# Kernel optimization log

Measured on AMD Instinct MI355X. Metric: run time of the kernel, lower is better.

The kernel has to match this reference:

```python
import jax, jax.numpy as jnp
import numpy as np

BCE_W, AMP_W, SMOOTH_W = 1.0, 0.5, 0.3
BIG = 1e30  # finite sentinel for masked min/max (avoids inf-inf NaNs)


def setup_inputs() -> dict:
    key = jax.random.key(0)
    k1, k2, k3 = jax.random.split(key, 3)
    B, L = 128, 100000
    signals = jax.random.normal(k1, (B, 1, L), dtype=jnp.float32)
    predictions = jax.random.normal(k2, (B, L, 1), dtype=jnp.float32)
    targets = jax.random.uniform(k3, (B, L, 1), dtype=jnp.float32)
    return {"signals": signals, "predictions": predictions, "targets": targets}


def _window_amp(mask, s, idx, L):
    # mask: [B, L] bool; s: [B, L] signal. Amplitude of s over [min_idx, max_idx].
    lo = jnp.min(jnp.where(mask, idx, L), axis=1)    # [B]
    hi = jnp.max(jnp.where(mask, idx, -1), axis=1)   # [B]
    w = (idx[None, :] >= lo[:, None]) & (idx[None, :] <= hi[:, None])  # [B, L]
    amp = jnp.max(jnp.where(w, s, -BIG), axis=1) - jnp.min(jnp.where(w, s, BIG), axis=1)
    return amp, jnp.any(mask, axis=1)


def reference(signals, predictions, targets):
    # predictions/targets: [B, L, 1] (3D path of the torch module)
    p, t = predictions, targets
    pred_sigmoid = jax.nn.sigmoid(p)
    # BCEWithLogitsLoss (mean), numerically stable
    bce_loss = jnp.mean(jnp.maximum(p, 0.0) - p * t + jnp.log1p(jnp.exp(-jnp.abs(p))))

    B, L = signals.shape[0], signals.shape[2]
    s = signals[:, 0, :]                              # [B, L]
    idx = jnp.arange(L)

    true_amp, t_has = _window_amp(t[:, :, 0] > 0.5, s, idx, L)
    pred_amp, p_has = _window_amp(pred_sigmoid[:, :, 0] > 0.5, s, idx, L)
    valid = t_has & p_has

    d = jnp.abs(true_amp - pred_amp)
    per = jnp.where(true_amp > 1e-6, d / (true_amp + 1e-6), d)
    amp_loss = jnp.sum(jnp.where(valid, per, 0.0)) / B

    # smoothness: mean |diff(pred_sigmoid, axis=1)|; L >= 2 so never empty
    smoothness_loss = jnp.mean(jnp.abs(pred_sigmoid[:, 1:, :] - pred_sigmoid[:, :-1, :]))

    return BCE_W * bce_loss + AMP_W * amp_loss + SMOOTH_W * smoothness_loss
```

## Files before the change

kernel.cpp:

```cpp
#include <hip/hip_runtime.h>
#include <math.h>
#include <float.h>

#define BATCH 128
#define LEN   100000
#define CHUNK 5000
#define SEGS  (LEN / CHUNK)
#define VPS   (CHUNK / 4)

struct WS {
    int*   lt_tab; int* ht_tab; int* lp_tab; int* hp_tab;
    float* bce_blk; float* sm_blk;
    float* cmin; float* cmax;
    float* wmn; float* wmx;
};

static inline WS ws_layout(void* d_ws) {
    WS w;
    w.lt_tab  = (int*)d_ws;
    w.ht_tab  = w.lt_tab + BATCH * SEGS;
    w.lp_tab  = w.ht_tab + BATCH * SEGS;
    w.hp_tab  = w.lp_tab + BATCH * SEGS;
    w.bce_blk = (float*)(w.hp_tab + BATCH * SEGS);
    w.sm_blk  = w.bce_blk + BATCH * SEGS;
    w.cmin    = w.sm_blk  + BATCH * SEGS;
    w.cmax    = w.cmin    + BATCH * SEGS;
    w.wmn     = w.cmax    + BATCH * SEGS;
    w.wmx     = w.wmn     + 2 * BATCH;
    return w;
}


__global__ __launch_bounds__(256) void k_main(
        const float* __restrict__ sig,
        const float* __restrict__ pred,
        const float* __restrict__ targ,
        int* __restrict__ lt_tab, int* __restrict__ ht_tab,
        int* __restrict__ lp_tab, int* __restrict__ hp_tab,
        float* __restrict__ bce_blk, float* __restrict__ sm_blk,
        float* __restrict__ cmin_tab, float* __restrict__ cmax_tab) {
    const int b   = blockIdx.y;
    const int seg = blockIdx.x;
    const int tid = threadIdx.x;
    const size_t row = (size_t)b * LEN;
    const float* prow = pred + row;
    const float* trow = targ + row;
    const float* srow = sig  + row;
    const int seg0 = seg * CHUNK;

    float bce = 0.0f, sm = 0.0f;
    float cmn = FLT_MAX, cmx = -FLT_MAX;
    int lt = LEN, ht = -1, lp = LEN, hp = -1;

    auto proc = [&](const float4& pv, const float4& tv, const float4& sv, int l0) {
        float sg0, sg1, sg2, sg3;
        #define ONE_ELEM(pp, tt, ss, sgv, ll) { \
            const float ap = fabsf(pp); \
            const float ee = __expf(-ap); \
            const float zz = 1.0f + ee; \
            const float rr = __builtin_amdgcn_rcpf(zz); \
            bce += fmaxf(pp, 0.0f) - (pp) * (tt) + __logf(zz); \
            sgv = ((pp) >= 0.0f) ? rr : ee * rr; \
            if ((tt) > 0.5f) { lt = min(lt, (ll)); ht = max(ht, (ll)); } \
            if ((pp) > 0.0f) { lp = min(lp, (ll)); hp = max(hp, (ll)); } \
            cmn = fminf(cmn, (ss)); cmx = fmaxf(cmx, (ss)); }
        ONE_ELEM(pv.x, tv.x, sv.x, sg0, l0 + 0)
        ONE_ELEM(pv.y, tv.y, sv.y, sg1, l0 + 1)
        ONE_ELEM(pv.z, tv.z, sv.z, sg2, l0 + 2)
        ONE_ELEM(pv.w, tv.w, sv.w, sg3, l0 + 3)
        #undef ONE_ELEM
        sm += fabsf(sg1 - sg0) + fabsf(sg2 - sg1) + fabsf(sg3 - sg2);
        const float prev3 = __shfl_up(sg3, 1);
        if ((tid & 63) == 0) {
            if (l0 > 0) {
                const float pp = prow[l0 - 1];
                const float ee = __expf(-fabsf(pp));
                const float rr = __builtin_amdgcn_rcpf(1.0f + ee);
                const float sp = (pp >= 0.0f) ? rr : ee * rr;
                sm += fabsf(sg0 - sp);
            }
        } else {
            sm += fabsf(sg0 - prev3);
        }
    };

    for (int vv = tid; vv < VPS; vv += 512) {
        const int l0 = seg0 + vv * 4;
        const float4 pv0 = *reinterpret_cast<const float4*>(prow + l0);
        const float4 tv0 = *reinterpret_cast<const float4*>(trow + l0);
        const float4 sv0 = *reinterpret_cast<const float4*>(srow + l0);
        const int vv2 = vv + 256;
        const bool h2 = (vv2 < VPS);
        const int l1 = seg0 + vv2 * 4;
        float4 pv1, tv1, sv1;
        if (h2) {
            pv1 = *reinterpret_cast<const float4*>(prow + l1);
            tv1 = *reinterpret_cast<const float4*>(trow + l1);
            sv1 = *reinterpret_cast<const float4*>(srow + l1);
        }
        proc(pv0, tv0, sv0, l0);
        if (h2) proc(pv1, tv1, sv1, l1);
    }

    #pragma unroll
    for (int o = 32; o > 0; o >>= 1) {
        bce += __shfl_xor(bce, o);
        sm  += __shfl_xor(sm,  o);
        cmn  = fminf(cmn, __shfl_xor(cmn, o));
        cmx  = fmaxf(cmx, __shfl_xor(cmx, o));
        lt   = min(lt, __shfl_xor(lt, o));
        ht   = max(ht, __shfl_xor(ht, o));
        lp   = min(lp, __shfl_xor(lp, o));
        hp   = max(hp, __shfl_xor(hp, o));
    }

    __shared__ float s_bce[4], s_sm[4], s_mn[4], s_mx[4];
    __shared__ int   s_lt[4], s_ht[4], s_lp[4], s_hp[4];
    const int w = tid >> 6, lane = tid & 63;
    if (lane == 0) {
        s_bce[w] = bce; s_sm[w] = sm; s_mn[w] = cmn; s_mx[w] = cmx;
        s_lt[w] = lt; s_ht[w] = ht; s_lp[w] = lp; s_hp[w] = hp;
    }
    __syncthreads();
    if (tid == 0) {
        float B = 0.0f, S = 0.0f, MN = FLT_MAX, MX = -FLT_MAX;
        int LT = LEN, HT = -1, LP = LEN, HP = -1;
        #pragma unroll
        for (int i = 0; i < 4; ++i) {
            B += s_bce[i]; S += s_sm[i];
            MN = fminf(MN, s_mn[i]); MX = fmaxf(MX, s_mx[i]);
            LT = min(LT, s_lt[i]); HT = max(HT, s_ht[i]);
            LP = min(LP, s_lp[i]); HP = max(HP, s_hp[i]);
        }
        const int e = b * SEGS + seg;
        bce_blk[e] = B; sm_blk[e] = S;
        cmin_tab[e] = MN; cmax_tab[e] = MX;
        lt_tab[e] = LT; ht_tab[e] = HT;
        lp_tab[e] = LP; hp_tab[e] = HP;
    }
}


__global__ __launch_bounds__(256) void k_rows(
        const float* __restrict__ sig,
        const int* __restrict__ lt_tab, const int* __restrict__ ht_tab,
        const int* __restrict__ lp_tab, const int* __restrict__ hp_tab,
        const float* __restrict__ cmin_tab, const float* __restrict__ cmax_tab,
        float* __restrict__ wmn, float* __restrict__ wmx) {
    const int b     = blockIdx.x;
    const int which = blockIdx.y;
    const int tid   = threadIdx.x;
    const int* lo_tab = which ? lp_tab : lt_tab;
    const int* hi_tab = which ? hp_tab : ht_tab;

    int lo = LEN, hi = -1;
    if (tid < SEGS) { lo = lo_tab[b * SEGS + tid]; hi = hi_tab[b * SEGS + tid]; }
    #pragma unroll
    for (int o = 32; o > 0; o >>= 1) {
        lo = min(lo, __shfl_xor(lo, o));
        hi = max(hi, __shfl_xor(hi, o));
    }
    __shared__ int s_lo, s_hi;
    if (tid == 0) { s_lo = lo; s_hi = hi; }
    __syncthreads();
    lo = s_lo; hi = s_hi;

    float mn = FLT_MAX, mx = -FLT_MAX;
    if (lo < LEN) {
        const float* srow = sig + (size_t)b * LEN;
        const int cl = lo / CHUNK, ch = hi / CHUNK;
        const int e1 = (cl == ch) ? hi : cl * CHUNK + CHUNK - 1;
        for (int l = lo + tid; l <= e1; l += 256) {
            const float x = srow[l]; mn = fminf(mn, x); mx = fmaxf(mx, x);
        }
        if (ch > cl) {
            for (int l = ch * CHUNK + tid; l <= hi; l += 256) {
                const float x = srow[l]; mn = fminf(mn, x); mx = fmaxf(mx, x);
            }
            const float* cmin_row = cmin_tab + b * SEGS;
            const float* cmax_row = cmax_tab + b * SEGS;
            for (int c = cl + 1 + tid; c < ch; c += 256) {
                mn = fminf(mn, cmin_row[c]); mx = fmaxf(mx, cmax_row[c]);
            }
        }
    }
    #pragma unroll
    for (int o = 32; o > 0; o >>= 1) {
        mn = fminf(mn, __shfl_xor(mn, o));
        mx = fmaxf(mx, __shfl_xor(mx, o));
    }
    __shared__ float sh_mn[4], sh_mx[4];
    const int w = tid >> 6, lane = tid & 63;
    if (lane == 0) { sh_mn[w] = mn; sh_mx[w] = mx; }
    __syncthreads();
    if (tid == 0) {
        float MN = fminf(fminf(sh_mn[0], sh_mn[1]), fminf(sh_mn[2], sh_mn[3]));
        float MX = fmaxf(fmaxf(sh_mx[0], sh_mx[1]), fmaxf(sh_mx[2], sh_mx[3]));
        if (lo >= LEN) { MN = 1e30f; MX = -1e30f; }
        wmn[which * BATCH + b] = MN;
        wmx[which * BATCH + b] = MX;
    }
}


__global__ void k_combine(const float* __restrict__ bce_blk,
                          const float* __restrict__ sm_blk,
                          const float* __restrict__ wmn,
                          const float* __restrict__ wmx,
                          float* __restrict__ out) {
    const int tid = threadIdx.x;
    float acc_b = 0.0f, acc_s = 0.0f, acc_a = 0.0f;
    for (int i = tid; i < BATCH * SEGS; i += 256) { acc_b += bce_blk[i]; acc_s += sm_blk[i]; }
    if (tid < BATCH) {
        const float tmn = wmn[tid],          tmx = wmx[tid];
        const float pmn = wmn[BATCH + tid],  pmx = wmx[BATCH + tid];
        if (tmx >= tmn && pmx >= pmn) {
            const float ta = tmx - tmn;
            const float pa = pmx - pmn;
            const float d  = fabsf(ta - pa);
            acc_a = (ta > 1e-6f) ? d / (ta + 1e-6f) : d;
        }
    }
    #pragma unroll
    for (int o = 32; o > 0; o >>= 1) {
        acc_b += __shfl_xor(acc_b, o);
        acc_s += __shfl_xor(acc_s, o);
        acc_a += __shfl_xor(acc_a, o);
    }
    __shared__ float sb[4], ss[4], sa[4];
    const int w = tid >> 6, lane = tid & 63;
    if (lane == 0) { sb[w] = acc_b; ss[w] = acc_s; sa[w] = acc_a; }
    __syncthreads();
    if (tid == 0) {
        const double B = (double)(sb[0] + sb[1] + sb[2] + sb[3]);
        const double S = (double)(ss[0] + ss[1] + ss[2] + ss[3]);
        const double A = (double)(sa[0] + sa[1] + sa[2] + sa[3]);
        const double bce = B / ((double)BATCH * (double)LEN);
        const double smo = S / ((double)BATCH * (double)(LEN - 1));
        const double amp = A / (double)BATCH;
        out[0] = (float)(1.0 * bce + 0.5 * amp + 0.3 * smo);
    }
}


extern "C" void kernel_launch(void* const* d_in, const int* in_sizes, int n_in,
                              void* d_out, int out_size, void* d_ws, size_t ws_size,
                              hipStream_t stream) {
    const float* signals = (const float*)d_in[0];
    const float* preds   = (const float*)d_in[1];
    const float* targs   = (const float*)d_in[2];
    float* out = (float*)d_out;
    WS w = ws_layout(d_ws);

    dim3 gm(SEGS, BATCH);
    k_main<<<gm, 256, 0, stream>>>(signals, preds, targs,
                                   w.lt_tab, w.ht_tab, w.lp_tab, w.hp_tab,
                                   w.bce_blk, w.sm_blk, w.cmin, w.cmax);

    dim3 gr(BATCH, 2);
    k_rows<<<gr, 256, 0, stream>>>(signals,
                                   w.lt_tab, w.ht_tab, w.lp_tab, w.hp_tab,
                                   w.cmin, w.cmax, w.wmn, w.wmx);

    k_combine<<<1, 256, 0, stream>>>(w.bce_blk, w.sm_blk, w.wmn, w.wmx, out);
}
```

Baseline: 48.92 us.

## Preload all per-thread chunk data up front and track indices via bitmasks

Replaces the strided loop with a fully unrolled structure. Each thread issues all five float4 loads per input, plus the wave-boundary predecessor loads, before any compute, so more memory requests are in flight. Per-element min/max index updates become bitmask ORs, and first/last indices are recovered at the end with ffs/clz. A launch-bounds occupancy hint is added; the extra held registers (60 floats of loaded data) may limit occupancy.

```diff
diff --git a/kernel.cpp b/kernel.cpp
--- a/kernel.cpp
+++ b/kernel.cpp
@@ -7,6 +7,7 @@
 #define CHUNK 5000
 #define SEGS  (LEN / CHUNK)
 #define VPS   (CHUNK / 4)
+#define NG    5
 
 struct WS {
     int*   lt_tab; int* ht_tab; int* lp_tab; int* hp_tab;
@@ -31,7 +32,7 @@
 }
 
 
-__global__ __launch_bounds__(256) void k_main(
+__global__ __launch_bounds__(256, 2) void k_main(
         const float* __restrict__ sig,
         const float* __restrict__ pred,
         const float* __restrict__ targ,
@@ -47,33 +48,60 @@
     const float* trow = targ + row;
     const float* srow = sig  + row;
     const int seg0 = seg * CHUNK;
+    const bool g4 = (tid < (VPS - 4 * 256));
+
+    float4 pv[NG], tv[NG], sv[NG];
+    #pragma unroll
+    for (int k = 0; k < NG; ++k) {
+        if (k < NG - 1 || g4) {
+            const int l0 = seg0 + (tid + k * 256) * 4;
+            pv[k] = *reinterpret_cast<const float4*>(prow + l0);
+            tv[k] = *reinterpret_cast<const float4*>(trow + l0);
+            sv[k] = *reinterpret_cast<const float4*>(srow + l0);
+        }
+    }
+    float pm[NG];
+    #pragma unroll
+    for (int k = 0; k < NG; ++k) {
+        pm[k] = 0.0f;
+        if (((tid & 63) == 0) && (k < NG - 1 || g4)) {
+            const int l0 = seg0 + (tid + k * 256) * 4;
+            if (l0 > 0) pm[k] = prow[l0 - 1];
+        }
+    }
 
     float bce = 0.0f, sm = 0.0f;
     float cmn = FLT_MAX, cmx = -FLT_MAX;
-    int lt = LEN, ht = -1, lp = LEN, hp = -1;
-
-    auto proc = [&](const float4& pv, const float4& tv, const float4& sv, int l0) {
+    unsigned tmask = 0u, pmask = 0u;
+
+    #pragma unroll
+    for (int k = 0; k < NG; ++k) {
+        if (k == NG - 1 && !g4) continue;
+        const float4 p4 = pv[k];
+        const float4 t4 = tv[k];
+        const float4 s4 = sv[k];
+        const int l0 = seg0 + (tid + k * 256) * 4;
         float sg0, sg1, sg2, sg3;
-        #define ONE_ELEM(pp, tt, ss, sgv, ll) { \
+        #define ONE_ELEM(pp, tt, ss, sgv, BIT) { \
             const float ap = fabsf(pp); \
             const float ee = __expf(-ap); \
             const float zz = 1.0f + ee; \
             const float rr = __builtin_amdgcn_rcpf(zz); \
             bce += fmaxf(pp, 0.0f) - (pp) * (tt) + __logf(zz); \
             sgv = ((pp) >= 0.0f) ? rr : ee * rr; \
-            if ((tt) > 0.5f) { lt = min(lt, (ll)); ht = max(ht, (ll)); } \
-            if ((pp) > 0.0f) { lp = min(lp, (ll)); hp = max(hp, (ll)); } \
+            tmask |= ((tt) > 0.5f) ? (1u << (BIT)) : 0u; \
+            pmask |= ((pp) > 0.0f) ? (1u << (BIT)) : 0u; \
             cmn = fminf(cmn, (ss)); cmx = fmaxf(cmx, (ss)); }
-        ONE_ELEM(pv.x, tv.x, sv.x, sg0, l0 + 0)
-        ONE_ELEM(pv.y, tv.y, sv.y, sg1, l0 + 1)
-        ONE_ELEM(pv.z, tv.z, sv.z, sg2, l0 + 2)
-        ONE_ELEM(pv.w, tv.w, sv.w, sg3, l0 + 3)
+        ONE_ELEM(p4.x, t4.x, s4.x, sg0, 4 * k + 0)
+        ONE_ELEM(p4.y, t4.y, s4.y, sg1, 4 * k + 1)
+        ONE_ELEM(p4.z, t4.z, s4.z, sg2, 4 * k + 2)
+        ONE_ELEM(p4.w, t4.w, s4.w, sg3, 4 * k + 3)
         #undef ONE_ELEM
         sm += fabsf(sg1 - sg0) + fabsf(sg2 - sg1) + fabsf(sg3 - sg2);
         const float prev3 = __shfl_up(sg3, 1);
         if ((tid & 63) == 0) {
             if (l0 > 0) {
-                const float pp = prow[l0 - 1];
+                const float pp = pm[k];
                 const float ee = __expf(-fabsf(pp));
                 const float rr = __builtin_amdgcn_rcpf(1.0f + ee);
                 const float sp = (pp >= 0.0f) ? rr : ee * rr;
@@ -82,24 +110,20 @@
         } else {
             sm += fabsf(sg0 - prev3);
         }
-    };
-
-    for (int vv = tid; vv < VPS; vv += 512) {
-        const int l0 = seg0 + vv * 4;
-        const float4 pv0 = *reinterpret_cast<const float4*>(prow + l0);
-        const float4 tv0 = *reinterpret_cast<const float4*>(trow + l0);
-        const float4 sv0 = *reinterpret_cast<const float4*>(srow + l0);
-        const int vv2 = vv + 256;
-        const bool h2 = (vv2 < VPS);
-        const int l1 = seg0 + vv2 * 4;
-        float4 pv1, tv1, sv1;
-        if (h2) {
-            pv1 = *reinterpret_cast<const float4*>(prow + l1);
-            tv1 = *reinterpret_cast<const float4*>(trow + l1);
-            sv1 = *reinterpret_cast<const float4*>(srow + l1);
-        }
-        proc(pv0, tv0, sv0, l0);
-        if (h2) proc(pv1, tv1, sv1, l1);
+    }
+
+    int lt = LEN, ht = -1, lp = LEN, hp = -1;
+    if (tmask) {
+        const int f = __ffs(tmask) - 1;
+        const int h = 31 - __clz((int)tmask);
+        lt = seg0 + (tid + (f >> 2) * 256) * 4 + (f & 3);
+        ht = seg0 + (tid + (h >> 2) * 256) * 4 + (h & 3);
+    }
+    if (pmask) {
+        const int f = __ffs(pmask) - 1;
+        const int h = 31 - __clz((int)pmask);
+        lp = seg0 + (tid + (f >> 2) * 256) * 4 + (f & 3);
+        hp = seg0 + (tid + (h >> 2) * 256) * 4 + (h & 3);
     }
 
     #pragma unroll
```

Result: no change. 48.92 us (+0.0%).
